# Performance work log

Hardware: AMD Instinct MI355X
Metric: run time of the kernel (lower is better)

The kernel has to match this reference:

```python
import jax, jax.numpy as jnp
import numpy as np

N_NODES = 100_000
N_EDGES = 1_200_000
N_GRAPHS = 256
HIT_IN, VAR_IN = 5, 19
H = 64            # hit_embed_dim (h_feat of ResGCN)
D = 128           # transformer hidden = hit + var embed
N_GNN, N_ENC, HEADS, NCLS = 6, 6, 8, 2
EPS = 1e-7        # GENConv message eps


def _ln(x, g, b, eps=1e-5):
    m = jnp.mean(x, -1, keepdims=True)
    v = jnp.mean((x - m) ** 2, -1, keepdims=True)
    return (x - m) * jax.lax.rsqrt(v + eps) * g + b


def _forward(floats, edge_index, batch):
    (x, var_data, enc_W, enc_b, ln_g, ln_b, t_param, mlp1_W, mlp1_b,
     mlpn_g, mlpn_b, mlp2_W, mlp2_b, v1_W, v1_b, v2_W, v2_b, v3_W, v3_b,
     qkv_W, qkv_b, out_W, out_b, ln1_g, ln1_b, ff1_W, ff1_b, ff2_W, ff2_b,
     ln2_g, ln2_b, head_W, head_b) = floats
    src, dst = edge_index[0], edge_index[1]
    N = x.shape[0]
    h = x @ enc_W + enc_b                                   # [N, H]
    for i in range(N_GNN):
        # DeepGCNLayer block='res+': norm -> relu -> conv, then residual add
        z = jax.nn.relu(_ln(h, ln_g[i], ln_b[i]))
        # GENConv aggr='softmax': per-channel segment softmax over incoming edges
        msg = jax.nn.relu(z[src]) + EPS                     # [E, H]
        s = msg * t_param[i]
        m = jax.lax.stop_gradient(jax.ops.segment_max(s, dst, num_segments=N))
        m = jnp.where(jnp.isfinite(m), m, 0.0)
        e = jnp.exp(s - m[dst])
        den = jax.ops.segment_sum(e, dst, num_segments=N)
        alpha = e / jnp.maximum(den, 1e-16)[dst]
        agg = jax.ops.segment_sum(msg * alpha, dst, num_segments=N)
        # GENConv: out = mlp(agg + x_dst); MLP = Lin(H,2H)->LN->ReLU->Lin(2H,H)
        u = z + agg
        u = jax.nn.relu(_ln(u @ mlp1_W[i] + mlp1_b[i], mlpn_g[i], mlpn_b[i]))
        u = u @ mlp2_W[i] + mlp2_b[i]
        h = h + u
    pooled = jax.ops.segment_sum(h, batch, num_segments=N_GRAPHS)  # [B, H]
    # VariableEmbed MLP 19->16->32->64
    v = jax.nn.relu(var_data @ v1_W + v1_b)
    v = jax.nn.relu(v @ v2_W + v2_b)
    v = v @ v3_W + v3_b
    # reshape(-1,1,D) -> seq_len = num_graphs, batch = 1 (post-norm encoder)
    t = jnp.concatenate([pooled, v], -1)                    # [B, D]
    S = t.shape[0]
    dh = D // HEADS
    for i in range(N_ENC):
        qkv = t @ qkv_W[i] + qkv_b[i]
        q, k, vv = jnp.split(qkv, 3, axis=-1)
        q = q.reshape(S, HEADS, dh).transpose(1, 0, 2)
        k = k.reshape(S, HEADS, dh).transpose(1, 0, 2)
        vv = vv.reshape(S, HEADS, dh).transpose(1, 0, 2)
        att = jax.nn.softmax(jnp.einsum('hqd,hkd->hqk', q, k) / jnp.sqrt(jnp.float32(dh)), axis=-1)
        o = jnp.einsum('hqk,hkd->hqd', att, vv).transpose(1, 0, 2).reshape(S, D)
        o = o @ out_W[i] + out_b[i]
        t = _ln(t + o, ln1_g[i], ln1_b[i])
        f = jax.nn.gelu(t @ ff1_W[i] + ff1_b[i], approximate=False)
        f = f @ ff2_W[i] + ff2_b[i]
        t = _ln(t + f, ln2_g[i], ln2_b[i])
    return t @ head_W + head_b                              # [B, NCLS]


FLOAT_KEYS = ['x', 'var_data', 'enc_W', 'enc_b', 'ln_g', 'ln_b', 't_param',
              'mlp1_W', 'mlp1_b', 'mlpn_g', 'mlpn_b', 'mlp2_W', 'mlp2_b',
              'v1_W', 'v1_b', 'v2_W', 'v2_b', 'v3_W', 'v3_b',
              'qkv_W', 'qkv_b', 'out_W', 'out_b', 'ln1_g', 'ln1_b',
              'ff1_W', 'ff1_b', 'ff2_W', 'ff2_b', 'ln2_g', 'ln2_b',
              'head_W', 'head_b']


def setup_inputs() -> dict:
    key = jax.random.key(0)
    ks = iter(jax.random.split(key, 64))
    def nrm(shape, s=0.05):
        return jax.random.normal(next(ks), shape, jnp.float32) * s
    return {
        'x': jax.random.normal(next(ks), (N_NODES, HIT_IN), jnp.float32),
        'edge_index': jax.random.randint(next(ks), (2, N_EDGES), 0, N_NODES),
        'batch': jnp.sort(jax.random.randint(next(ks), (N_NODES,), 0, N_GRAPHS)),
        'var_data': jax.random.normal(next(ks), (N_GRAPHS, VAR_IN), jnp.float32),
        'enc_W': nrm((HIT_IN, H)), 'enc_b': jnp.zeros((H,)),
        'ln_g': jnp.ones((N_GNN, H)), 'ln_b': jnp.zeros((N_GNN, H)),
        't_param': jnp.ones((N_GNN,)),
        'mlp1_W': nrm((N_GNN, H, 2 * H)), 'mlp1_b': jnp.zeros((N_GNN, 2 * H)),
        'mlpn_g': jnp.ones((N_GNN, 2 * H)), 'mlpn_b': jnp.zeros((N_GNN, 2 * H)),
        'mlp2_W': nrm((N_GNN, 2 * H, H)), 'mlp2_b': jnp.zeros((N_GNN, H)),
        'v1_W': nrm((VAR_IN, 16)), 'v1_b': jnp.zeros((16,)),
        'v2_W': nrm((16, 32)), 'v2_b': jnp.zeros((32,)),
        'v3_W': nrm((32, 64)), 'v3_b': jnp.zeros((64,)),
        'qkv_W': nrm((N_ENC, D, 3 * D)), 'qkv_b': jnp.zeros((N_ENC, 3 * D)),
        'out_W': nrm((N_ENC, D, D)), 'out_b': jnp.zeros((N_ENC, D)),
        'ln1_g': jnp.ones((N_ENC, D)), 'ln1_b': jnp.zeros((N_ENC, D)),
        'ff1_W': nrm((N_ENC, D, D)), 'ff1_b': jnp.zeros((N_ENC, D)),
        'ff2_W': nrm((N_ENC, D, D)), 'ff2_b': jnp.zeros((N_ENC, D)),
        'ln2_g': jnp.ones((N_ENC, D)), 'ln2_b': jnp.zeros((N_ENC, D)),
        'head_W': nrm((D, NCLS)), 'head_b': jnp.zeros((NCLS,)),
    }


def reference(x, edge_index, batch, var_data, enc_W, enc_b, ln_g, ln_b, t_param,
              mlp1_W, mlp1_b, mlpn_g, mlpn_b, mlp2_W, mlp2_b,
              v1_W, v1_b, v2_W, v2_b, v3_W, v3_b,
              qkv_W, qkv_b, out_W, out_b, ln1_g, ln1_b,
              ff1_W, ff1_b, ff2_W, ff2_b, ln2_g, ln2_b, head_W, head_b):
    floats = (x, var_data, enc_W, enc_b, ln_g, ln_b, t_param, mlp1_W, mlp1_b,
              mlpn_g, mlpn_b, mlp2_W, mlp2_b, v1_W, v1_b, v2_W, v2_b, v3_W, v3_b,
              qkv_W, qkv_b, out_W, out_b, ln1_g, ln1_b, ff1_W, ff1_b, ff2_W, ff2_b,
              ln2_g, ln2_b, head_W, head_b)
    return _forward(floats, edge_index, batch)
```

## Files before the change

### kernel.cpp

```cpp
#include <hip/hip_runtime.h>
#include <hip/hip_bf16.h>
#include <math.h>

#define NODES 100000
#define EDGES 1200000
#define NG 256

typedef unsigned short u16;
typedef unsigned int   u32;
typedef __attribute__((ext_vector_type(8))) short bf16x8;
typedef __attribute__((ext_vector_type(4))) float f32x4;

__device__ __forceinline__ u16 f2bf(float f){
  u32 u = __float_as_uint(f);
  u32 r = (u + 0x7FFFu + ((u >> 16) & 1u)) >> 16;
  return (u16)r;
}
__device__ __forceinline__ float bf2f(u16 b){ return __uint_as_float(((u32)b) << 16); }
__device__ __forceinline__ float bfL(u32 v){ return __uint_as_float(v << 16); }
__device__ __forceinline__ float bfH(u32 v){ return __uint_as_float(v & 0xFFFF0000u); }
__device__ __forceinline__ u32 pk2(float a, float b){ return (u32)f2bf(a) | ((u32)f2bf(b) << 16); }

__device__ __forceinline__ float wsum64(float v){
  v += __shfl_xor(v, 32); v += __shfl_xor(v, 16); v += __shfl_xor(v, 8);
  v += __shfl_xor(v, 4);  v += __shfl_xor(v, 2);  v += __shfl_xor(v, 1);
  return v;
}
__device__ __forceinline__ float wmax64(float v){
  v = fmaxf(v, __shfl_xor(v, 32)); v = fmaxf(v, __shfl_xor(v, 16));
  v = fmaxf(v, __shfl_xor(v, 8));  v = fmaxf(v, __shfl_xor(v, 4));
  v = fmaxf(v, __shfl_xor(v, 2));  v = fmaxf(v, __shfl_xor(v, 1));
  return v;
}
__device__ __forceinline__ float bsum256(float v, float* red){
  v = wsum64(v);
  if ((threadIdx.x & 63) == 0) red[threadIdx.x >> 6] = v;
  __syncthreads();
  float r = red[0] + red[1] + red[2] + red[3];
  __syncthreads();
  return r;
}

__global__ void k_init(int* counts, float* pooled,
                       const float* __restrict__ m1W, const float* __restrict__ m2W,
                       u16* __restrict__ w1t_g, u16* __restrict__ w2t_g){
  int idx = blockIdx.x*256 + threadIdx.x;
  if (idx < NODES) counts[idx] = 0;
  if (idx < NG*64) pooled[idx] = 0.f;
  if (idx < 49152){
    int L = idx >> 13, r = idx & 8191, j = r >> 6, k = r & 63;
    w1t_g[idx] = f2bf(m1W[(L << 13) + k*128 + j]);
  }
  if (idx < 98304 && idx >= 49152){
    int t = idx - 49152;
    int L = t >> 13, r = t & 8191, j = r >> 7, k = r & 127;
    w2t_g[t] = f2bf(m2W[(L << 13) + k*64 + j]);
  }
}

__global__ void k_hist(const int* __restrict__ dst, int* __restrict__ counts){
  int e = blockIdx.x*256 + threadIdx.x;
  if (e < EDGES) atomicAdd(&counts[dst[e]], 1);
}

__global__ void k_scan1(const int* __restrict__ counts, int* __restrict__ rowptr, int* __restrict__ bsums){
  __shared__ int sd[256];
  int tid = threadIdx.x;
  int base = blockIdx.x*2048 + tid*8;
  int v[8]; int s = 0;
  #pragma unroll
  for (int i = 0; i < 8; i++){
    int idx = base + i;
    int c = (idx < NODES) ? counts[idx] : 0;
    v[i] = s; s += c;
  }
  sd[tid] = s;
  __syncthreads();
  for (int off = 1; off < 256; off <<= 1){
    int t = 0;
    if (tid >= off) t = sd[tid - off];
    __syncthreads();
    if (tid >= off) sd[tid] += t;
    __syncthreads();
  }
  int excl = (tid > 0) ? sd[tid-1] : 0;
  #pragma unroll
  for (int i = 0; i < 8; i++){
    int idx = base + i;
    if (idx < NODES) rowptr[idx] = v[i] + excl;
  }
  if (tid == 255) bsums[blockIdx.x] = sd[255];
}

__global__ void k_scan2(const int* __restrict__ bsums, int* __restrict__ boffs, int nb){
  int tid = threadIdx.x;
  int acc = 0;
  for (int j = 0; j < nb; j++){
    int b = bsums[j];
    if (j < tid) acc += b;
  }
  if (tid < nb) boffs[tid] = acc;
}

__global__ void k_scan3(int* __restrict__ rowptr, int* __restrict__ cursor, const int* __restrict__ boffs){
  int i = blockIdx.x*256 + threadIdx.x;
  if (i < NODES){
    int r = rowptr[i] + boffs[i >> 11];
    rowptr[i] = r; cursor[i] = r;
  }
  if (i == 0) rowptr[NODES] = EDGES;
}

__global__ void k_scatter(const int* __restrict__ src, const int* __restrict__ dst,
                          int* __restrict__ cursor, int* __restrict__ esrc){
  int e = blockIdx.x*256 + threadIdx.x;
  if (e < EDGES){
    int d = dst[e];
    int p = atomicAdd(&cursor[d], 1);
    esrc[p] = src[e];
  }
}

__global__ __launch_bounds__(256) void k_enc(const float* __restrict__ x,
    const float* __restrict__ encW, const float* __restrict__ encb,
    const float* __restrict__ lg, const float* __restrict__ lb,
    u16* __restrict__ hbf, u16* __restrict__ z){
  __shared__ float we[320], wb[64], sg[64], sb[64];
  int tid = threadIdx.x;
  for (int i = tid; i < 320; i += 256) we[i] = encW[i];
  if (tid < 64){ wb[tid] = encb[tid]; sg[tid] = lg[tid]; sb[tid] = lb[tid]; }
  __syncthreads();
  int n = blockIdx.x*256 + tid;
  if (n >= NODES) return;
  float xv[5];
  #pragma unroll
  for (int k = 0; k < 5; k++) xv[k] = x[n*5 + k];
  float a[64];
  #pragma unroll
  for (int c = 0; c < 64; c++){
    float t = wb[c];
    #pragma unroll
    for (int k = 0; k < 5; k++) t += xv[k]*we[k*64 + c];
    a[c] = t;
  }
  float mean = 0.f;
  #pragma unroll
  for (int c = 0; c < 64; c++) mean += a[c];
  mean *= (1.f/64.f);
  float var = 0.f;
  #pragma unroll
  for (int c = 0; c < 64; c++){ float d = a[c]-mean; var += d*d; }
  var *= (1.f/64.f);
  float rstd = rsqrtf(var + 1e-5f);
  size_t rb = (size_t)n*64;
  #pragma unroll
  for (int c = 0; c < 64; c += 4){
    uint2 hv;
    hv.x = pk2(a[c], a[c+1]); hv.y = pk2(a[c+2], a[c+3]);
    *(uint2*)&hbf[rb + c] = hv;
    uint2 zv;
    zv.x = pk2(fmaxf((a[c  ]-mean)*rstd*sg[c  ]+sb[c  ], 0.f),
               fmaxf((a[c+1]-mean)*rstd*sg[c+1]+sb[c+1], 0.f));
    zv.y = pk2(fmaxf((a[c+2]-mean)*rstd*sg[c+2]+sb[c+2], 0.f),
               fmaxf((a[c+3]-mean)*rstd*sg[c+3]+sb[c+3], 0.f));
    *(uint2*)&z[rb + c] = zv;
  }
}

__global__ __launch_bounds__(256) void k_agg(const u32* __restrict__ z32, u32* __restrict__ uo,
    const int* __restrict__ rowptr, const int* __restrict__ esrc,
    const float* __restrict__ tparam, int li){
  int lane = threadIdx.x & 63;
  int q  = lane >> 4;
  int cl = lane & 15;
  int n = blockIdx.x*16 + (threadIdx.x >> 6)*4 + q;
  if (n >= NODES) return;
  float tp = tparam[li];
  int beg = rowptr[n], end = rowptr[n+1];
  const uint2* zq = (const uint2*)z32;
  uint2 zp = zq[(size_t)n*16 + cl];
  float zn0 = bfL(zp.x), zn1 = bfH(zp.x), zn2 = bfL(zp.y), zn3 = bfH(zp.y);
  float den0=0.f,num0=0.f,den1=0.f,num1=0.f,den2=0.f,num2=0.f,den3=0.f,num3=0.f;
  int e = beg;
  for (; e + 7 < end; e += 8){
    int si[8];
    #pragma unroll
    for (int r = 0; r < 8; r++) si[r] = esrc[e + r];
    uint2 vv[8];
    #pragma unroll
    for (int r = 0; r < 8; r++) vv[r] = zq[(size_t)si[r]*16 + cl];
    #pragma unroll
    for (int r = 0; r < 8; r++){
      float m0 = bfL(vv[r].x) + 1e-7f, m1 = bfH(vv[r].x) + 1e-7f;
      float m2 = bfL(vv[r].y) + 1e-7f, m3 = bfH(vv[r].y) + 1e-7f;
      float e0 = __expf(m0*tp), e1 = __expf(m1*tp), e2 = __expf(m2*tp), e3 = __expf(m3*tp);
      den0 += e0; num0 += m0*e0;
      den1 += e1; num1 += m1*e1;
      den2 += e2; num2 += m2*e2;
      den3 += e3; num3 += m3*e3;
    }
  }
  for (; e + 3 < end; e += 4){
    int si[4];
    #pragma unroll
    for (int r = 0; r < 4; r++) si[r] = esrc[e + r];
    uint2 vv[4];
    #pragma unroll
    for (int r = 0; r < 4; r++) vv[r] = zq[(size_t)si[r]*16 + cl];
    #pragma unroll
    for (int r = 0; r < 4; r++){
      float m0 = bfL(vv[r].x) + 1e-7f, m1 = bfH(vv[r].x) + 1e-7f;
      float m2 = bfL(vv[r].y) + 1e-7f, m3 = bfH(vv[r].y) + 1e-7f;
      float e0 = __expf(m0*tp), e1 = __expf(m1*tp), e2 = __expf(m2*tp), e3 = __expf(m3*tp);
      den0 += e0; num0 += m0*e0;
      den1 += e1; num1 += m1*e1;
      den2 += e2; num2 += m2*e2;
      den3 += e3; num3 += m3*e3;
    }
  }
  for (; e < end; ++e){
    uint2 v = zq[(size_t)esrc[e]*16 + cl];
    float m0 = bfL(v.x) + 1e-7f, m1 = bfH(v.x) + 1e-7f;
    float m2 = bfL(v.y) + 1e-7f, m3 = bfH(v.y) + 1e-7f;
    float e0 = __expf(m0*tp), e1 = __expf(m1*tp), e2 = __expf(m2*tp), e3 = __expf(m3*tp);
    den0 += e0; num0 += m0*e0;
    den1 += e1; num1 += m1*e1;
    den2 += e2; num2 += m2*e2;
    den3 += e3; num3 += m3*e3;
  }
  uint2 o;
  o.x = pk2(zn0 + num0 / fmaxf(den0, 1e-16f), zn1 + num1 / fmaxf(den1, 1e-16f));
  o.y = pk2(zn2 + num2 / fmaxf(den2, 1e-16f), zn3 + num3 / fmaxf(den3, 1e-16f));
  ((uint2*)uo)[(size_t)n*16 + cl] = o;
}

__global__ __launch_bounds__(256) void k_mlpm(
    const u16* __restrict__ u, u16* __restrict__ hbf, u16* __restrict__ znext,
    float* __restrict__ pooled, const int* __restrict__ batch,
    const u16* __restrict__ w1t_g, const u16* __restrict__ w2t_g,
    const float* __restrict__ B1, const float* __restrict__ G1, const float* __restrict__ Q1,
    const float* __restrict__ B2, const float* __restrict__ GN, const float* __restrict__ BN,
    int last){
  __shared__ u16 w1t[128*88];
  __shared__ u16 w2t[64*152];
  __shared__ float cb1[128], cg1[128], cq1[128];
  __shared__ float cb2[64], cgn[64], cbn[64];
  int tid = threadIdx.x;
  const uint4* w1g = (const uint4*)w1t_g;
  const uint4* w2g = (const uint4*)w2t_g;
  for (int i = tid; i < 1024; i += 256){
    { int j = i >> 3, c = i & 7;  *(uint4*)&w1t[j*88  + c*8] = w1g[i]; }
    { int j = i >> 4, c = i & 15; *(uint4*)&w2t[j*152 + c*8] = w2g[i]; }
  }
  if (tid < 128){ cb1[tid] = B1[tid]; cg1[tid] = G1[tid]; cq1[tid] = Q1[tid]; }
  if (tid < 64){
    cb2[tid] = B2[tid];
    cgn[tid] = last ? 0.f : GN[tid];
    cbn[tid] = last ? 0.f : BN[tid];
  }
  __syncthreads();

  int w = tid >> 6, l = tid & 63, l15 = l & 15, g = l >> 4;
  int nd = w*16 + l15;
  int base0 = blockIdx.x*128;
  int hi = g >> 1;
  int s0l = ((g & 1) << 5) + l15;
  int s1l = s0l + 16;
  f32x4 zero4 = {0.f, 0.f, 0.f, 0.f};
  bf16x8 bz8 = {0,0,0,0,0,0,0,0};

  bf16x8 buA[2], buB[2];
  #pragma unroll
  for (int it = 0; it < 2; it++){
    int node = base0 + it*64 + nd;
    bool ok = node < NODES;
    buA[it] = ok ? *(const bf16x8*)&u[(size_t)node*64 +      g*8] : bz8;
    buB[it] = ok ? *(const bf16x8*)&u[(size_t)node*64 + 32 + g*8] : bz8;
  }

  #pragma unroll
  for (int it = 0; it < 2; it++){
    int node = base0 + it*64 + nd;
    bool ok = node < NODES;
    f32x4 c1[8];
    #pragma unroll
    for (int mt = 0; mt < 8; mt++) c1[mt] = zero4;
    #pragma unroll
    for (int mt = 0; mt < 8; mt++){
      bf16x8 aw0 = *(const bf16x8*)&w1t[(mt*16 + l15)*88 +      g*8];
      c1[mt] = __builtin_amdgcn_mfma_f32_16x16x32_bf16(aw0, buA[it], c1[mt], 0, 0, 0);
      bf16x8 aw1 = *(const bf16x8*)&w1t[(mt*16 + l15)*88 + 32 + g*8];
      c1[mt] = __builtin_amdgcn_mfma_f32_16x16x32_bf16(aw1, buB[it], c1[mt], 0, 0, 0);
    }
    float sum = 0.f, sq = 0.f;
    #pragma unroll
    for (int mt = 0; mt < 8; mt++){
      #pragma unroll
      for (int r = 0; r < 4; r++){
        float v = c1[mt][r] + cb1[mt*16 + g*4 + r];
        c1[mt][r] = v;
        sum += v; sq += v*v;
      }
    }
    sum += __shfl_xor(sum, 16); sum += __shfl_xor(sum, 32);
    sq  += __shfl_xor(sq, 16);  sq  += __shfl_xor(sq, 32);
    float mean = sum*(1.f/128.f);
    float var  = sq*(1.f/128.f) - mean*mean;
    float rstd = rsqrtf(fmaxf(var, 0.f) + 1e-5f);
    u32 pk0[8], pk1[8];
    #pragma unroll
    for (int mt = 0; mt < 8; mt++){
      int ch = mt*16 + g*4;
      float a0 = fmaxf((c1[mt][0]-mean)*rstd*cg1[ch  ] + cq1[ch  ], 0.f);
      float a1 = fmaxf((c1[mt][1]-mean)*rstd*cg1[ch+1] + cq1[ch+1], 0.f);
      float a2 = fmaxf((c1[mt][2]-mean)*rstd*cg1[ch+2] + cq1[ch+2], 0.f);
      float a3 = fmaxf((c1[mt][3]-mean)*rstd*cg1[ch+3] + cq1[ch+3], 0.f);
      pk0[mt] = pk2(a0, a1);
      pk1[mt] = pk2(a2, a3);
    }
    f32x4 c2[4];
    #pragma unroll
    for (int mt = 0; mt < 4; mt++) c2[mt] = zero4;
    #pragma unroll
    for (int ks = 0; ks < 4; ks++){
      u32 x0 = pk0[2*ks], x1 = pk0[2*ks+1];
      u32 y0 = pk1[2*ks], y1 = pk1[2*ks+1];
      u32 a0 = (u32)__shfl((int)x0, s0l), a1 = (u32)__shfl((int)x1, s0l);
      u32 b0 = (u32)__shfl((int)y0, s0l), b1 = (u32)__shfl((int)y1, s0l);
      u32 c0 = (u32)__shfl((int)x0, s1l), c1v = (u32)__shfl((int)x1, s1l);
      u32 d0 = (u32)__shfl((int)y0, s1l), d1 = (u32)__shfl((int)y1, s1l);
      union { u32 q[4]; bf16x8 v; } bb;
      bb.q[0] = hi ? a1 : a0;
      bb.q[1] = hi ? b1 : b0;
      bb.q[2] = hi ? c1v : c0;
      bb.q[3] = hi ? d1 : d0;
      #pragma unroll
      for (int mt = 0; mt < 4; mt++){
        bf16x8 aw = *(const bf16x8*)&w2t[(mt*16 + l15)*152 + ks*32 + g*8];
        c2[mt] = __builtin_amdgcn_mfma_f32_16x16x32_bf16(aw, bb.v, c2[mt], 0, 0, 0);
      }
    }
    if (ok){
      float out[16];
      size_t hb = (size_t)node*64;
      #pragma unroll
      for (int mt = 0; mt < 4; mt++){
        int ch = mt*16 + g*4;
        uint2 hv = *(const uint2*)&hbf[hb + ch];
        out[mt*4  ] = c2[mt][0] + cb2[ch  ] + bfL(hv.x);
        out[mt*4+1] = c2[mt][1] + cb2[ch+1] + bfH(hv.x);
        out[mt*4+2] = c2[mt][2] + cb2[ch+2] + bfL(hv.y);
        out[mt*4+3] = c2[mt][3] + cb2[ch+3] + bfH(hv.y);
      }
      if (!last){
        #pragma unroll
        for (int mt = 0; mt < 4; mt++){
          int ch = mt*16 + g*4;
          uint2 hv;
          hv.x = pk2(out[mt*4  ], out[mt*4+1]);
          hv.y = pk2(out[mt*4+2], out[mt*4+3]);
          *(uint2*)&hbf[hb + ch] = hv;
        }
        float s2 = 0.f, q2 = 0.f;
        #pragma unroll
        for (int c = 0; c < 16; c++){ s2 += out[c]; q2 += out[c]*out[c]; }
        s2 += __shfl_xor(s2, 16); s2 += __shfl_xor(s2, 32);
        q2 += __shfl_xor(q2, 16); q2 += __shfl_xor(q2, 32);
        float m2 = s2*(1.f/64.f);
        float v2 = q2*(1.f/64.f) - m2*m2;
        float rs2 = rsqrtf(fmaxf(v2, 0.f) + 1e-5f);
        #pragma unroll
        for (int mt = 0; mt < 4; mt++){
          int ch = mt*16 + g*4;
          uint2 pk;
          pk.x = pk2(fmaxf((out[mt*4  ]-m2)*rs2*cgn[ch  ] + cbn[ch  ], 0.f),
                     fmaxf((out[mt*4+1]-m2)*rs2*cgn[ch+1] + cbn[ch+1], 0.f));
          pk.y = pk2(fmaxf((out[mt*4+2]-m2)*rs2*cgn[ch+2] + cbn[ch+2], 0.f),
                     fmaxf((out[mt*4+3]-m2)*rs2*cgn[ch+3] + cbn[ch+3], 0.f));
          *(uint2*)&znext[hb + ch] = pk;
        }
      } else {
        int gb = batch[node];
        #pragma unroll
        for (int c = 0; c < 16; c++){
          int ch = (c >> 2)*16 + g*4 + (c & 3);
          atomicAdd(&pooled[gb*64 + ch], out[c]);
        }
      }
    }
  }
}

__global__ __launch_bounds__(128) void k_pool2(
    const float* __restrict__ pooled, const float* __restrict__ var_data,
    const float* __restrict__ v1W, const float* __restrict__ v1b,
    const float* __restrict__ v2W, const float* __restrict__ v2b,
    const float* __restrict__ v3W, const float* __restrict__ v3b,
    float* __restrict__ t, u16* __restrict__ qkvout,
    const float* __restrict__ qW, const float* __restrict__ qb){
  __shared__ float vin[19], l1[16], l2[32], tr[128];
  int c = threadIdx.x, s = blockIdx.x;
  if (c < 19) vin[c] = var_data[s*19 + c];
  __syncthreads();
  if (c < 16){
    float a = v1b[c];
    for (int k = 0; k < 19; k++) a += vin[k]*v1W[k*16 + c];
    l1[c] = fmaxf(a, 0.f);
  }
  __syncthreads();
  if (c < 32){
    float a = v2b[c];
    for (int k = 0; k < 16; k++) a += l1[k]*v2W[k*32 + c];
    l2[c] = fmaxf(a, 0.f);
  }
  __syncthreads();
  float tv;
  if (c < 64) tv = pooled[s*64 + c];
  else {
    float a = v3b[c-64];
    for (int k = 0; k < 32; k++) a += l2[k]*v3W[k*64 + (c-64)];
    tv = a;
  }
  tr[c] = tv; t[s*128 + c] = tv;
  __syncthreads();
  #pragma unroll 1
  for (int r = 0; r < 3; r++){
    int col = r*128 + c;
    float a = qb[col];
    #pragma unroll 4
    for (int k = 0; k < 128; k++) a += tr[k]*qW[k*384 + col];
    qkvout[s*384 + col] = f2bf(a);
  }
}

__global__ __launch_bounds__(256) void k_attrow(
    const u16* __restrict__ qkv, float* __restrict__ t, u16* __restrict__ qkvout,
    const float* __restrict__ outW, const float* __restrict__ outb,
    const float* __restrict__ l1g, const float* __restrict__ l1b,
    const float* __restrict__ f1W, const float* __restrict__ f1b,
    const float* __restrict__ f2W, const float* __restrict__ f2b,
    const float* __restrict__ l2g, const float* __restrict__ l2b,
    const float* __restrict__ qW, const float* __restrict__ qb,
    const float* __restrict__ hW, const float* __restrict__ hb2,
    float* __restrict__ dout, int last){
  __shared__ float kv[8448];
  __shared__ float sc[8*260];
  __shared__ float qrow[128], orow[128], strow[128], s1row[128], sfrow[128], t2row[128];
  __shared__ float red[4];
  int tid = threadIdx.x, s = blockIdx.x;
  const u32* qkv32 = (const u32*)qkv;
  if (tid < 128){ qrow[tid] = bf2f(qkv[(size_t)s*384 + tid]); strow[tid] = t[(size_t)s*128 + tid]; }
  for (int tile = 0; tile < 4; tile++){
    __syncthreads();
    for (int i = tid; i < 4096; i += 256){
      int r = i >> 6, c2 = i & 63;
      u32 v = qkv32[(size_t)(tile*64 + r)*192 + 64 + c2];
      kv[r*132 + c2*2    ] = bfL(v);
      kv[r*132 + c2*2 + 1] = bfH(v);
    }
    __syncthreads();
    int j = tid >> 2, sub = tid & 3;
    float d0 = 0.f, d1 = 0.f;
    #pragma unroll
    for (int d = 0; d < 16; d++){
      d0 += qrow[sub*16 + d]     * kv[j*132 + sub*16 + d];
      d1 += qrow[(sub+4)*16 + d] * kv[j*132 + (sub+4)*16 + d];
    }
    sc[sub*260     + tile*64 + j] = d0*0.25f;
    sc[(sub+4)*260 + tile*64 + j] = d1*0.25f;
  }
  __syncthreads();
  {
    int wid = tid >> 6, lane = tid & 63;
    #pragma unroll
    for (int hh = 0; hh < 2; hh++){
      int hh2 = wid*2 + hh;
      float a0 = sc[hh2*260 + lane], a1 = sc[hh2*260 + 64 + lane];
      float a2 = sc[hh2*260 + 128 + lane], a3 = sc[hh2*260 + 192 + lane];
      float m = wmax64(fmaxf(fmaxf(a0,a1), fmaxf(a2,a3)));
      float e0 = __expf(a0-m), e1 = __expf(a1-m), e2 = __expf(a2-m), e3 = __expf(a3-m);
      float sum = wsum64((e0+e1)+(e2+e3));
      float inv = 1.f/sum;
      sc[hh2*260 + lane] = e0*inv; sc[hh2*260 + 64 + lane] = e1*inv;
      sc[hh2*260 + 128 + lane] = e2*inv; sc[hh2*260 + 192 + lane] = e3*inv;
    }
  }
  float o = 0.f;
  int hme = (tid & 127) >> 4;
  for (int tile = 0; tile < 4; tile++){
    __syncthreads();
    for (int i = tid; i < 4096; i += 256){
      int r = i >> 6, c2 = i & 63;
      u32 v = qkv32[(size_t)(tile*64 + r)*192 + 128 + c2];
      kv[r*132 + c2*2    ] = bfL(v);
      kv[r*132 + c2*2 + 1] = bfH(v);
    }
    __syncthreads();
    if (tid < 128){
      #pragma unroll 4
      for (int j = 0; j < 64; j++)
        o += sc[hme*260 + tile*64 + j] * kv[j*132 + tid];
    }
  }
  if (tid < 128) orow[tid] = o;
  float acc = (tid < 128) ? outb[tid] : 0.f;
  for (int kt = 0; kt < 4; kt++){
    __syncthreads();
    for (int i = tid; i < 4096; i += 256) kv[i] = outW[(size_t)kt*4096 + i];
    __syncthreads();
    if (tid < 128){
      #pragma unroll 8
      for (int kk = 0; kk < 32; kk++) acc += orow[kt*32 + kk]*kv[kk*128 + tid];
    }
  }
  if (tid < 128) acc += strow[tid];
  float mean = bsum256((tid < 128) ? acc : 0.f, red)*(1.f/128.f);
  float d0v = (tid < 128) ? (acc - mean) : 0.f;
  float var = bsum256(d0v*d0v, red)*(1.f/128.f);
  float t1 = 0.f;
  if (tid < 128){
    t1 = d0v*rsqrtf(var + 1e-5f)*l1g[tid] + l1b[tid];
    s1row[tid] = t1;
  }
  float f = (tid < 128) ? f1b[tid] : 0.f;
  for (int kt = 0; kt < 4; kt++){
    __syncthreads();
    for (int i = tid; i < 4096; i += 256) kv[i] = f1W[(size_t)kt*4096 + i];
    __syncthreads();
    if (tid < 128){
      #pragma unroll 8
      for (int kk = 0; kk < 32; kk++) f += s1row[kt*32 + kk]*kv[kk*128 + tid];
    }
  }
  if (tid < 128){
    f = 0.5f*f*(1.f + erff(f*0.70710678118654752f));
    sfrow[tid] = f;
  }
  float g = (tid < 128) ? f2b[tid] : 0.f;
  for (int kt = 0; kt < 4; kt++){
    __syncthreads();
    for (int i = tid; i < 4096; i += 256) kv[i] = f2W[(size_t)kt*4096 + i];
    __syncthreads();
    if (tid < 128){
      #pragma unroll 8
      for (int kk = 0; kk < 32; kk++) g += sfrow[kt*32 + kk]*kv[kk*128 + tid];
    }
  }
  if (tid < 128) g += t1;
  float mean2 = bsum256((tid < 128) ? g : 0.f, red)*(1.f/128.f);
  float d2v = (tid < 128) ? (g - mean2) : 0.f;
  float var2 = bsum256(d2v*d2v, red)*(1.f/128.f);
  if (tid < 128){
    float t2 = d2v*rsqrtf(var2 + 1e-5f)*l2g[tid] + l2b[tid];
    t[(size_t)s*128 + tid] = t2;
    t2row[tid] = t2;
  }
  __syncthreads();
  if (!last){
    float a0 = qb[tid];
    float a1 = (tid < 128) ? qb[256 + tid] : 0.f;
    for (int kt = 0; kt < 8; kt++){
      __syncthreads();
      for (int i = tid; i < 6144; i += 256) kv[i] = qW[(size_t)kt*6144 + i];
      __syncthreads();
      #pragma unroll 4
      for (int kk = 0; kk < 16; kk++){
        float tv = t2row[kt*16 + kk];
        a0 += tv*kv[kk*384 + tid];
        if (tid < 128) a1 += tv*kv[kk*384 + 256 + tid];
      }
    }
    qkvout[(size_t)s*384 + tid] = f2bf(a0);
    if (tid < 128) qkvout[(size_t)s*384 + 256 + tid] = f2bf(a1);
  } else {
    if (tid < 2){
      float a = hb2[tid];
      for (int k = 0; k < 128; k++) a += t2row[k]*hW[k*2 + tid];
      dout[s*2 + tid] = a;
    }
  }
}

extern "C" void kernel_launch(void* const* d_in, const int* in_sizes, int n_in,
                              void* d_out, int out_size, void* d_ws, size_t ws_size,
                              hipStream_t stream){
  const float* x       = (const float*)d_in[0];
  const int*   ei      = (const int*)  d_in[1];
  const int*   batch   = (const int*)  d_in[2];
  const float* var_d   = (const float*)d_in[3];
  const float* encW    = (const float*)d_in[4];
  const float* encb    = (const float*)d_in[5];
  const float* ln_g    = (const float*)d_in[6];
  const float* ln_b    = (const float*)d_in[7];
  const float* tparam  = (const float*)d_in[8];
  const float* m1W     = (const float*)d_in[9];
  const float* m1b     = (const float*)d_in[10];
  const float* mng     = (const float*)d_in[11];
  const float* mnb     = (const float*)d_in[12];
  const float* m2W     = (const float*)d_in[13];
  const float* m2b     = (const float*)d_in[14];
  const float* v1W     = (const float*)d_in[15];
  const float* v1b     = (const float*)d_in[16];
  const float* v2W     = (const float*)d_in[17];
  const float* v2b     = (const float*)d_in[18];
  const float* v3W     = (const float*)d_in[19];
  const float* v3b     = (const float*)d_in[20];
  const float* qkvW    = (const float*)d_in[21];
  const float* qkvB    = (const float*)d_in[22];
  const float* outW    = (const float*)d_in[23];
  const float* outb    = (const float*)d_in[24];
  const float* l1g     = (const float*)d_in[25];
  const float* l1b     = (const float*)d_in[26];
  const float* f1W     = (const float*)d_in[27];
  const float* f1b     = (const float*)d_in[28];
  const float* f2W     = (const float*)d_in[29];
  const float* f2b     = (const float*)d_in[30];
  const float* l2g     = (const float*)d_in[31];
  const float* l2b     = (const float*)d_in[32];
  const float* headW   = (const float*)d_in[33];
  const float* headB   = (const float*)d_in[34];
  float* dout = (float*)d_out;

  char* wsb = (char*)d_ws;
  size_t off = 0;
  auto nxt = [&](size_t bytes)->void*{
    void* p = wsb + off;
    off += (bytes + 255) & ~(size_t)255;
    return p;
  };
  u16*   h      = (u16*)  nxt((size_t)NODES*64*2);
  u16*   z      = (u16*)  nxt((size_t)NODES*64*2);
  u16*   u      = (u16*)  nxt((size_t)NODES*64*2);
  int*   rowptr = (int*)  nxt((size_t)(NODES+1)*4);
  int*   cursor = (int*)  nxt((size_t)NODES*4);
  int*   counts = (int*)  nxt((size_t)NODES*4);
  int*   bsums  = (int*)  nxt(64*4);
  int*   boffs  = (int*)  nxt(64*4);
  int*   esrc   = (int*)  nxt((size_t)EDGES*4);
  float* pooled = (float*)nxt((size_t)NG*64*4);
  float* tbuf   = (float*)nxt((size_t)NG*128*4);
  u16*   qkv0   = (u16*)  nxt((size_t)NG*384*2);
  u16*   qkv1   = (u16*)  nxt((size_t)NG*384*2);
  u16*   w1tg   = (u16*)  nxt((size_t)49152*2);
  u16*   w2tg   = (u16*)  nxt((size_t)49152*2);
  u16*   qkvb[2] = { qkv0, qkv1 };

  const int* srcp = ei;
  const int* dstp = ei + EDGES;

  k_init   <<<391, 256, 0, stream>>>(counts, pooled, m1W, m2W, w1tg, w2tg);
  k_hist   <<<4688, 256, 0, stream>>>(dstp, counts);
  k_scan1  <<<49, 256, 0, stream>>>(counts, rowptr, bsums);
  k_scan2  <<<1, 64, 0, stream>>>(bsums, boffs, 49);
  k_scan3  <<<391, 256, 0, stream>>>(rowptr, cursor, boffs);
  k_scatter<<<4688, 256, 0, stream>>>(srcp, dstp, cursor, esrc);
  k_enc    <<<391, 256, 0, stream>>>(x, encW, encb, ln_g, ln_b, h, z);

  for (int i = 0; i < 6; i++){
    int last = (i == 5);
    k_agg <<<6250, 256, 0, stream>>>((const u32*)z, (u32*)u, rowptr, esrc, tparam, i);
    k_mlpm<<<782, 256, 0, stream>>>(u, h, z, pooled, batch,
        w1tg + i*8192, w2tg + i*8192,
        m1b + i*128, mng + i*128, mnb + i*128,
        m2b + i*64,
        ln_g + (last ? 0 : (i+1)*64), ln_b + (last ? 0 : (i+1)*64), last);
  }

  k_pool2<<<NG, 128, 0, stream>>>(pooled, var_d, v1W, v1b, v2W, v2b, v3W, v3b,
                                  tbuf, qkv0, qkvW, qkvB);

  for (int i = 0; i < 6; i++){
    int last = (i == 5);
    k_attrow<<<NG, 256, 0, stream>>>(qkvb[i & 1], tbuf, qkvb[(i + 1) & 1],
        outW + i*16384, outb + i*128, l1g + i*128, l1b + i*128,
        f1W + i*16384, f1b + i*128, f2W + i*16384, f2b + i*128,
        l2g + i*128, l2b + i*128,
        qkvW + (size_t)(last ? 0 : (i+1))*49152, qkvB + (last ? 0 : (i+1))*384,
        headW, headB, dout, last);
  }
}
```

Before: 1.444 ms.

## Process eight sequence rows per block in transformer encoder kernel

The fused attention/FFN kernel now handles 8 query rows per block instead of one, launching 32 blocks instead of 256. Each K/V tile and weight tile staged in shared memory is reused across 8 rows, which cuts redundant global loads and staging work. LayerNorms become per-wave reductions over rows. In exchange, far fewer blocks run on the GPU, so parallelism drops and per-block register and shared memory use grows.

```diff
diff --git a/kernel.cpp b/kernel.cpp
--- a/kernel.cpp
+++ b/kernel.cpp
@@ -31,14 +31,6 @@
   v = fmaxf(v, __shfl_xor(v, 8));  v = fmaxf(v, __shfl_xor(v, 4));
   v = fmaxf(v, __shfl_xor(v, 2));  v = fmaxf(v, __shfl_xor(v, 1));
   return v;
-}
-__device__ __forceinline__ float bsum256(float v, float* red){
-  v = wsum64(v);
-  if ((threadIdx.x & 63) == 0) red[threadIdx.x >> 6] = v;
-  __syncthreads();
-  float r = red[0] + red[1] + red[2] + red[3];
-  __syncthreads();
-  return r;
 }
 
 __global__ void k_init(int* counts, float* pooled,
@@ -443,140 +435,206 @@
     const float* __restrict__ qW, const float* __restrict__ qb,
     const float* __restrict__ hW, const float* __restrict__ hb2,
     float* __restrict__ dout, int last){
-  __shared__ float kv[8448];
-  __shared__ float sc[8*260];
-  __shared__ float qrow[128], orow[128], strow[128], s1row[128], sfrow[128], t2row[128];
-  __shared__ float red[4];
-  int tid = threadIdx.x, s = blockIdx.x;
+  __shared__ float kvw[8448];
+  __shared__ float sc[8*2080];
+  __shared__ float qr[8*132], st[8*132], orw[8*132], s1[8*132], sf[8*132], t2[8*132];
+  int tid = threadIdx.x;
+  int rb = blockIdx.x*8;
   const u32* qkv32 = (const u32*)qkv;
-  if (tid < 128){ qrow[tid] = bf2f(qkv[(size_t)s*384 + tid]); strow[tid] = t[(size_t)s*128 + tid]; }
+  for (int i = tid; i < 1024; i += 256){
+    int r = i >> 7, c = i & 127;
+    qr[r*132 + c] = bf2f(qkv[(size_t)(rb + r)*384 + c]);
+    st[r*132 + c] = t[(size_t)(rb + r)*128 + c];
+  }
+  int j = tid >> 2, sub = tid & 3;
   for (int tile = 0; tile < 4; tile++){
     __syncthreads();
     for (int i = tid; i < 4096; i += 256){
       int r = i >> 6, c2 = i & 63;
       u32 v = qkv32[(size_t)(tile*64 + r)*192 + 64 + c2];
-      kv[r*132 + c2*2    ] = bfL(v);
-      kv[r*132 + c2*2 + 1] = bfH(v);
-    }
-    __syncthreads();
-    int j = tid >> 2, sub = tid & 3;
-    float d0 = 0.f, d1 = 0.f;
-    #pragma unroll
-    for (int d = 0; d < 16; d++){
-      d0 += qrow[sub*16 + d]     * kv[j*132 + sub*16 + d];
-      d1 += qrow[(sub+4)*16 + d] * kv[j*132 + (sub+4)*16 + d];
-    }
-    sc[sub*260     + tile*64 + j] = d0*0.25f;
-    sc[(sub+4)*260 + tile*64 + j] = d1*0.25f;
+      kvw[r*132 + c2*2    ] = bfL(v);
+      kvw[r*132 + c2*2 + 1] = bfH(v);
+    }
+    __syncthreads();
+    #pragma unroll 1
+    for (int r = 0; r < 8; r++){
+      float d0 = 0.f, d1 = 0.f;
+      #pragma unroll
+      for (int d = 0; d < 16; d++){
+        d0 += qr[r*132 + sub*16 + d]     * kvw[j*132 + sub*16 + d];
+        d1 += qr[r*132 + (sub+4)*16 + d] * kvw[j*132 + (sub+4)*16 + d];
+      }
+      sc[r*2080 + sub*260     + tile*64 + j] = d0*0.25f;
+      sc[r*2080 + (sub+4)*260 + tile*64 + j] = d1*0.25f;
+    }
   }
   __syncthreads();
   {
-    int wid = tid >> 6, lane = tid & 63;
-    #pragma unroll
-    for (int hh = 0; hh < 2; hh++){
-      int hh2 = wid*2 + hh;
-      float a0 = sc[hh2*260 + lane], a1 = sc[hh2*260 + 64 + lane];
-      float a2 = sc[hh2*260 + 128 + lane], a3 = sc[hh2*260 + 192 + lane];
-      float m = wmax64(fmaxf(fmaxf(a0,a1), fmaxf(a2,a3)));
-      float e0 = __expf(a0-m), e1 = __expf(a1-m), e2 = __expf(a2-m), e3 = __expf(a3-m);
-      float sum = wsum64((e0+e1)+(e2+e3));
-      float inv = 1.f/sum;
-      sc[hh2*260 + lane] = e0*inv; sc[hh2*260 + 64 + lane] = e1*inv;
-      sc[hh2*260 + 128 + lane] = e2*inv; sc[hh2*260 + 192 + lane] = e3*inv;
-    }
-  }
-  float o = 0.f;
-  int hme = (tid & 127) >> 4;
+    int w = tid >> 6, lane = tid & 63;
+    #pragma unroll 1
+    for (int rr = 0; rr < 2; rr++){
+      int r = w*2 + rr;
+      #pragma unroll 1
+      for (int h2 = 0; h2 < 8; h2++){
+        float* sp = &sc[r*2080 + h2*260];
+        float a0 = sp[lane], a1 = sp[64 + lane], a2 = sp[128 + lane], a3 = sp[192 + lane];
+        float m = wmax64(fmaxf(fmaxf(a0,a1), fmaxf(a2,a3)));
+        float e0 = __expf(a0-m), e1 = __expf(a1-m), e2 = __expf(a2-m), e3 = __expf(a3-m);
+        float sum = wsum64((e0+e1)+(e2+e3));
+        float inv = 1.f/sum;
+        sp[lane] = e0*inv; sp[64 + lane] = e1*inv;
+        sp[128 + lane] = e2*inv; sp[192 + lane] = e3*inv;
+      }
+    }
+  }
+  int col = tid & 127, rg = tid >> 7;
+  int hme = col >> 4;
+  float o4[4] = {0.f, 0.f, 0.f, 0.f};
   for (int tile = 0; tile < 4; tile++){
     __syncthreads();
     for (int i = tid; i < 4096; i += 256){
       int r = i >> 6, c2 = i & 63;
       u32 v = qkv32[(size_t)(tile*64 + r)*192 + 128 + c2];
-      kv[r*132 + c2*2    ] = bfL(v);
-      kv[r*132 + c2*2 + 1] = bfH(v);
-    }
-    __syncthreads();
-    if (tid < 128){
-      #pragma unroll 4
-      for (int j = 0; j < 64; j++)
-        o += sc[hme*260 + tile*64 + j] * kv[j*132 + tid];
-    }
-  }
-  if (tid < 128) orow[tid] = o;
-  float acc = (tid < 128) ? outb[tid] : 0.f;
+      kvw[r*132 + c2*2    ] = bfL(v);
+      kvw[r*132 + c2*2 + 1] = bfH(v);
+    }
+    __syncthreads();
+    #pragma unroll 2
+    for (int jj = 0; jj < 64; jj++){
+      float vv = kvw[jj*132 + col];
+      #pragma unroll
+      for (int rr = 0; rr < 4; rr++)
+        o4[rr] += sc[(rg*4+rr)*2080 + hme*260 + tile*64 + jj] * vv;
+    }
+  }
+  #pragma unroll
+  for (int rr = 0; rr < 4; rr++) orw[(rg*4+rr)*132 + col] = o4[rr];
+  float acc[4];
+  #pragma unroll
+  for (int rr = 0; rr < 4; rr++) acc[rr] = outb[col];
   for (int kt = 0; kt < 4; kt++){
     __syncthreads();
-    for (int i = tid; i < 4096; i += 256) kv[i] = outW[(size_t)kt*4096 + i];
-    __syncthreads();
-    if (tid < 128){
-      #pragma unroll 8
-      for (int kk = 0; kk < 32; kk++) acc += orow[kt*32 + kk]*kv[kk*128 + tid];
-    }
-  }
-  if (tid < 128) acc += strow[tid];
-  float mean = bsum256((tid < 128) ? acc : 0.f, red)*(1.f/128.f);
-  float d0v = (tid < 128) ? (acc - mean) : 0.f;
-  float var = bsum256(d0v*d0v, red)*(1.f/128.f);
-  float t1 = 0.f;
-  if (tid < 128){
-    t1 = d0v*rsqrtf(var + 1e-5f)*l1g[tid] + l1b[tid];
-    s1row[tid] = t1;
-  }
-  float f = (tid < 128) ? f1b[tid] : 0.f;
+    for (int i = tid; i < 4096; i += 256) kvw[i] = outW[(size_t)kt*4096 + i];
+    __syncthreads();
+    #pragma unroll 4
+    for (int kk = 0; kk < 32; kk++){
+      float wv = kvw[kk*128 + col];
+      #pragma unroll
+      for (int rr = 0; rr < 4; rr++)
+        acc[rr] += orw[(rg*4+rr)*132 + kt*32 + kk] * wv;
+    }
+  }
+  #pragma unroll
+  for (int rr = 0; rr < 4; rr++)
+    s1[(rg*4+rr)*132 + col] = acc[rr] + st[(rg*4+rr)*132 + col];
+  __syncthreads();
+  {
+    int w = tid >> 6, lane = tid & 63;
+    #pragma unroll 1
+    for (int rr = 0; rr < 2; rr++){
+      int r = w*2 + rr;
+      float v0 = s1[r*132 + lane], v1 = s1[r*132 + 64 + lane];
+      float mean = wsum64(v0 + v1)*(1.f/128.f);
+      float d0 = v0 - mean, d1 = v1 - mean;
+      float var = wsum64(d0*d0 + d1*d1)*(1.f/128.f);
+      float rstd = rsqrtf(var + 1e-5f);
+      s1[r*132 + lane]      = d0*rstd*l1g[lane]      + l1b[lane];
+      s1[r*132 + 64 + lane] = d1*rstd*l1g[64 + lane] + l1b[64 + lane];
+    }
+  }
+  __syncthreads();
+  float f4[4];
+  #pragma unroll
+  for (int rr = 0; rr < 4; rr++) f4[rr] = f1b[col];
   for (int kt = 0; kt < 4; kt++){
     __syncthreads();
-    for (int i = tid; i < 4096; i += 256) kv[i] = f1W[(size_t)kt*4096 + i];
-    __syncthreads();
-    if (tid < 128){
-      #pragma unroll 8
-      for (int kk = 0; kk < 32; kk++) f += s1row[kt*32 + kk]*kv[kk*128 + tid];
-    }
-  }
-  if (tid < 128){
-    f = 0.5f*f*(1.f + erff(f*0.70710678118654752f));
-    sfrow[tid] = f;
-  }
-  float g = (tid < 128) ? f2b[tid] : 0.f;
+    for (int i = tid; i < 4096; i += 256) kvw[i] = f1W[(size_t)kt*4096 + i];
+    __syncthreads();
+    #pragma unroll 4
+    for (int kk = 0; kk < 32; kk++){
+      float wv = kvw[kk*128 + col];
+      #pragma unroll
+      for (int rr = 0; rr < 4; rr++)
+        f4[rr] += s1[(rg*4+rr)*132 + kt*32 + kk] * wv;
+    }
+  }
+  #pragma unroll
+  for (int rr = 0; rr < 4; rr++){
+    float fv = f4[rr];
+    sf[(rg*4+rr)*132 + col] = 0.5f*fv*(1.f + erff(fv*0.70710678118654752f));
+  }
+  __syncthreads();
+  float g4[4];
+  #pragma unroll
+  for (int rr = 0; rr < 4; rr++) g4[rr] = f2b[col];
   for (int kt = 0; kt < 4; kt++){
     __syncthreads();
-    for (int i = tid; i < 4096; i += 256) kv[i] = f2W[(size_t)kt*4096 + i];
-    __syncthreads();
-    if (tid < 128){
-      #pragma unroll 8
-      for (int kk = 0; kk < 32; kk++) g += sfrow[kt*32 + kk]*kv[kk*128 + tid];
-    }
-  }
-  if (tid < 128) g += t1;
-  float mean2 = bsum256((tid < 128) ? g : 0.f, red)*(1.f/128.f);
-  float d2v = (tid < 128) ? (g - mean2) : 0.f;
-  float var2 = bsum256(d2v*d2v, red)*(1.f/128.f);
-  if (tid < 128){
-    float t2 = d2v*rsqrtf(var2 + 1e-5f)*l2g[tid] + l2b[tid];
-    t[(size_t)s*128 + tid] = t2;
-    t2row[tid] = t2;
+    for (int i = tid; i < 4096; i += 256) kvw[i] = f2W[(size_t)kt*4096 + i];
+    __syncthreads();
+    #pragma unroll 4
+    for (int kk = 0; kk < 32; kk++){
+      float wv = kvw[kk*128 + col];
+      #pragma unroll
+      for (int rr = 0; rr < 4; rr++)
+        g4[rr] += sf[(rg*4+rr)*132 + kt*32 + kk] * wv;
+    }
+  }
+  #pragma unroll
+  for (int rr = 0; rr < 4; rr++)
+    t2[(rg*4+rr)*132 + col] = g4[rr] + s1[(rg*4+rr)*132 + col];
+  __syncthreads();
+  {
+    int w = tid >> 6, lane = tid & 63;
+    #pragma unroll 1
+    for (int rr = 0; rr < 2; rr++){
+      int r = w*2 + rr;
+      float v0 = t2[r*132 + lane], v1 = t2[r*132 + 64 + lane];
+      float mean = wsum64(v0 + v1)*(1.f/128.f);
+      float d0 = v0 - mean, d1 = v1 - mean;
+      float var = wsum64(d0*d0 + d1*d1)*(1.f/128.f);
+      float rstd = rsqrtf(var + 1e-5f);
+      float o0 = d0*rstd*l2g[lane]      + l2b[lane];
+      float o1 = d1*rstd*l2g[64 + lane] + l2b[64 + lane];
+      t2[r*132 + lane] = o0; t2[r*132 + 64 + lane] = o1;
+      t[(size_t)(rb + r)*128 + lane] = o0;
+      t[(size_t)(rb + r)*128 + 64 + lane] = o1;
+    }
   }
   __syncthreads();
   if (!last){
-    float a0 = qb[tid];
-    float a1 = (tid < 128) ? qb[256 + tid] : 0.f;
+    float a0[8], a1[8];
+    #pragma unroll
+    for (int r = 0; r < 8; r++){
+      a0[r] = qb[tid];
+      a1[r] = (tid < 128) ? qb[256 + tid] : 0.f;
+    }
     for (int kt = 0; kt < 8; kt++){
       __syncthreads();
-      for (int i = tid; i < 6144; i += 256) kv[i] = qW[(size_t)kt*6144 + i];
+      for (int i = tid; i < 6144; i += 256) kvw[i] = qW[(size_t)kt*6144 + i];
       __syncthreads();
-      #pragma unroll 4
+      #pragma unroll 2
       for (int kk = 0; kk < 16; kk++){
-        float tv = t2row[kt*16 + kk];
-        a0 += tv*kv[kk*384 + tid];
-        if (tid < 128) a1 += tv*kv[kk*384 + 256 + tid];
+        float w0 = kvw[kk*384 + tid];
+        float w1 = (tid < 128) ? kvw[kk*384 + 256 + tid] : 0.f;
+        #pragma unroll
+        for (int r = 0; r < 8; r++){
+          float tv = t2[r*132 + kt*16 + kk];
+          a0[r] += tv*w0;
+          a1[r] += tv*w1;
+        }
       }
     }
-    qkvout[(size_t)s*384 + tid] = f2bf(a0);
-    if (tid < 128) qkvout[(size_t)s*384 + 256 + tid] = f2bf(a1);
+    #pragma unroll
+    for (int r = 0; r < 8; r++){
+      qkvout[(size_t)(rb + r)*384 + tid] = f2bf(a0[r]);
+      if (tid < 128) qkvout[(size_t)(rb + r)*384 + 256 + tid] = f2bf(a1[r]);
+    }
   } else {
-    if (tid < 2){
-      float a = hb2[tid];
-      for (int k = 0; k < 128; k++) a += t2row[k]*hW[k*2 + tid];
-      dout[s*2 + tid] = a;
+    if (tid < 16){
+      int r = tid >> 1, c = tid & 1;
+      float a = hb2[c];
+      for (int k = 0; k < 128; k++) a += t2[r*132 + k]*hW[k*2 + c];
+      dout[(rb + r)*2 + c] = a;
     }
   }
 }
@@ -671,7 +729,7 @@
 
   for (int i = 0; i < 6; i++){
     int last = (i == 5);
-    k_attrow<<<NG, 256, 0, stream>>>(qkvb[i & 1], tbuf, qkvb[(i + 1) & 1],
+    k_attrow<<<32, 256, 0, stream>>>(qkvb[i & 1], tbuf, qkvb[(i + 1) & 1],
         outW + i*16384, outb + i*128, l1g + i*128, l1b + i*128,
         f1W + i*16384, f1b + i*128, f2W + i*16384, f2b + i*128,
         l2g + i*128, l2b + i*128,
```

Result: slower. 1.658 ms (+14.8%).
